# Performance work log

Measured on AMD Instinct MI355X. Metric: run time of the kernel, lower is better.

The kernel has to match this reference:

```python
import jax, jax.numpy as jnp
import numpy as np

B, T, D, H = 4, 1024, 1024, 16
DH = D // H
NEG_BIG = jnp.float32(-2.0**32 + 1)


def layer_norm(x, scale, bias, eps=1e-5):
    mean = jnp.mean(x, axis=-1, keepdims=True)
    var = jnp.mean(jnp.square(x - mean), axis=-1, keepdims=True)
    return (x - mean) * jax.lax.rsqrt(var + eps) * scale + bias


def setup_inputs() -> dict:
    key = jax.random.key(0)
    ks = jax.random.split(key, 10)
    s = 0.02
    x = jax.random.normal(ks[0], (B, T, D), jnp.float32)
    mask = jax.random.randint(ks[1], (B, T), 0, 2).astype(jnp.float32)
    return {
        "x": x,
        "mask": mask,
        "wq": jax.random.normal(ks[2], (D, D), jnp.float32) * s,
        "wk": jax.random.normal(ks[3], (D, D), jnp.float32) * s,
        "wv": jax.random.normal(ks[4], (D, D), jnp.float32) * s,
        "w1": jax.random.normal(ks[5], (D, D), jnp.float32) * s,
        "b1": jnp.zeros((D,), jnp.float32),
        "w2": jax.random.normal(ks[6], (D, D), jnp.float32) * s,
        "b2": jnp.zeros((D,), jnp.float32),
        "ln1_s": jnp.ones((D,), jnp.float32),
        "ln1_b": jnp.zeros((D,), jnp.float32),
        "ln2_s": jnp.ones((D,), jnp.float32),
        "ln2_b": jnp.zeros((D,), jnp.float32),
        "ln3_s": jnp.ones((D,), jnp.float32),
        "ln3_b": jnp.zeros((D,), jnp.float32),
    }


def _mask_enc(x, mask, wq, wk, wv, w1, b1, w2, b2,
              ln1_s, ln1_b, ln2_s, ln2_b, ln3_s, ln3_b):
    b, t, d = x.shape
    # --- multi-head attention (hand-rolled, matches torch split/cat trick) ---
    Q = (x @ wq).reshape(b, t, H, DH).transpose(0, 2, 1, 3)  # [B,H,T,dh]
    K = (x @ wk).reshape(b, t, H, DH).transpose(0, 2, 1, 3)
    V = (x @ wv).reshape(b, t, H, DH).transpose(0, 2, 1, 3)
    scores = jnp.einsum('bhqd,bhkd->bhqk', Q, K) / jnp.sqrt(jnp.float32(DH))
    # key padding mask from sign of |K| row sums
    key_m = jnp.sign(jnp.sum(jnp.abs(K), axis=-1))  # [B,H,T]
    scores = jnp.where(key_m[:, :, None, :] == 0, NEG_BIG, scores)
    # FORWARD direction: allowed where col_index > row_index (strict)
    idx = jnp.arange(t)
    allowed = (idx[None, :] > idx[:, None]).astype(scores.dtype)  # [T,T]
    scores = scores + (1.0 - allowed) * (-10000.0)
    attn = jax.nn.softmax(scores, axis=-1)
    # post-softmax query mask multiply
    query_m = jnp.sign(jnp.sum(jnp.abs(Q), axis=-1))[:, :, :, None]  # [B,H,T,1]
    attn = attn * query_m
    out = jnp.einsum('bhqk,bhkd->bhqd', attn, V)
    out = out.transpose(0, 2, 1, 3).reshape(b, t, d)  # combine heads
    out = out * mask[:, :, None]
    # --- residual + layernorm wrapper (attention) ---
    h1 = layer_norm(x + out, ln1_s, ln1_b)
    # --- FFN + residual + layernorm ---
    ffn = jax.nn.relu(h1 @ w1 + b1) @ w2 + b2
    h2 = layer_norm(h1 + ffn, ln2_s, ln2_b)
    # --- output normalization ---
    return layer_norm(h2, ln3_s, ln3_b)


def reference(x, mask, wq, wk, wv, w1, b1, w2, b2,
              ln1_s, ln1_b, ln2_s, ln2_b, ln3_s, ln3_b):
    return _mask_enc(x, mask, wq, wk, wv, w1, b1, w2, b2,
                     ln1_s, ln1_b, ln2_s, ln2_b, ln3_s, ln3_b)
```

## Files before the change

kernel.cpp:

```cpp
#include <hip/hip_runtime.h>
#include <stdint.h>


#define B_  4
#define T_  1024
#define D_  1024
#define H_  16
#define DH_ 64

typedef __attribute__((ext_vector_type(8))) short short8;
typedef __attribute__((ext_vector_type(4))) float floatx4;

__device__ __forceinline__ unsigned short f2bf(float f) {
  union { float f; uint32_t u; } a; a.f = f;
  uint32_t r = a.u + 0x7FFFu + ((a.u >> 16) & 1u);
  return (unsigned short)(r >> 16);
}
__device__ __forceinline__ float bf2f(unsigned short u) {
  union { uint32_t u; float f; } a; a.u = ((uint32_t)u) << 16;
  return a.f;
}

#define GLD_LDS16(g, l) __builtin_amdgcn_global_load_lds( \
    (const __attribute__((address_space(1))) unsigned int*)(g), \
    (__attribute__((address_space(3))) unsigned int*)(l), 16, 0, 0)

__global__ __launch_bounds__(256)
void cast_x_kernel(const float4* __restrict__ x4, unsigned short* __restrict__ xb) {
  int idx = blockIdx.x * 256 + threadIdx.x;
  float4 v = x4[idx];
  union { uint2 u; unsigned short s[4]; } o;
  o.s[0] = f2bf(v.x); o.s[1] = f2bf(v.y); o.s[2] = f2bf(v.z); o.s[3] = f2bf(v.w);
  *(uint2*)&xb[(size_t)idx * 4] = o.u;
}

__global__ __launch_bounds__(256)
void transpose_cast_w(const float* __restrict__ w0, const float* __restrict__ w1,
                      const float* __restrict__ w2, const float* __restrict__ w3,
                      const float* __restrict__ w4, unsigned short* __restrict__ dst_all) {
  const int z = blockIdx.z;
  const float* src = (z == 0) ? w0 : (z == 1) ? w1 : (z == 2) ? w2 : (z == 3) ? w3 : w4;
  unsigned short* dst = dst_all + (size_t)z * D_ * D_;
  __shared__ __align__(16) unsigned short tile[64 * 72];
  const int t = threadIdx.x;
  const int k0 = blockIdx.y * 64, n0 = blockIdx.x * 64;
#pragma unroll
  for (int c = 0; c < 4; ++c) {
    int idx = c * 256 + t;
    int r = idx >> 4, cc = (idx & 15) << 2;
    float4 v = *(const float4*)&src[(size_t)(k0 + r) * D_ + n0 + cc];
    tile[(cc + 0) * 72 + r] = f2bf(v.x);
    tile[(cc + 1) * 72 + r] = f2bf(v.y);
    tile[(cc + 2) * 72 + r] = f2bf(v.z);
    tile[(cc + 3) * 72 + r] = f2bf(v.w);
  }
  __syncthreads();
  int rr = t >> 2, ck = (t & 3) << 4;
  uint4 v0 = *(const uint4*)&tile[rr * 72 + ck];
  uint4 v1 = *(const uint4*)&tile[rr * 72 + ck + 8];
  *(uint4*)&dst[(size_t)(n0 + rr) * D_ + k0 + ck] = v0;
  *(uint4*)&dst[(size_t)(n0 + rr) * D_ + k0 + ck + 8] = v1;
}

__global__ __launch_bounds__(256, 2)
void gemm_qkv(const unsigned short* __restrict__ A,
              const unsigned short* __restrict__ Bt,
              unsigned short* __restrict__ oQ, unsigned short* __restrict__ oK,
              unsigned short* __restrict__ oV) {
  const int K = 1024;
  __shared__ __align__(16) unsigned short As[128 * 32];
  __shared__ __align__(16) unsigned short Bs[128 * 32];
  const int t = threadIdx.x;
  const int lane = t & 63, w = t >> 6;
  const int quad = lane >> 4, lm = lane & 15;
  const int wm = w >> 1, wn = w & 1;
  const int m0 = blockIdx.y * 128, n0 = blockIdx.x * 128;
  const int arow = w * 32 + (lane >> 2), acol = (lane & 3) << 3;

  floatx4 acc[4][4];
#pragma unroll
  for (int i = 0; i < 4; ++i)
#pragma unroll
    for (int j = 0; j < 4; ++j) acc[i][j] = (floatx4){0.f, 0.f, 0.f, 0.f};

  for (int kt = 0; kt < K; kt += 32) {
    const unsigned short* ga = A + (size_t)(m0 + arow) * K + kt + acol;
    const unsigned short* gb = Bt + (size_t)(n0 + arow) * K + kt + acol;
    GLD_LDS16(ga, &As[(w * 32) * 32]);
    GLD_LDS16(ga + (size_t)16 * K, &As[(w * 32 + 16) * 32]);
    GLD_LDS16(gb, &Bs[(w * 32) * 32]);
    GLD_LDS16(gb + (size_t)16 * K, &Bs[(w * 32 + 16) * 32]);
    __syncthreads();
    short8 a[4], b[4];
#pragma unroll
    for (int i = 0; i < 4; ++i) a[i] = *(const short8*)&As[(wm * 64 + i * 16 + lm) * 32 + quad * 8];
#pragma unroll
    for (int j = 0; j < 4; ++j) b[j] = *(const short8*)&Bs[(wn * 64 + j * 16 + lm) * 32 + quad * 8];
#pragma unroll
    for (int i = 0; i < 4; ++i)
#pragma unroll
      for (int j = 0; j < 4; ++j)
        acc[i][j] = __builtin_amdgcn_mfma_f32_16x16x32_bf16(a[i], b[j], acc[i][j], 0, 0, 0);
    __syncthreads();
  }

#pragma unroll
  for (int i = 0; i < 4; ++i) {
    int gmb = m0 + wm * 64 + i * 16 + quad * 4;
#pragma unroll
    for (int j = 0; j < 4; ++j) {
      int gn = n0 + wn * 64 + j * 16 + lm;
      int which = gn >> 10, nn = gn & 1023, hh = nn >> 6, dd = nn & 63;
#pragma unroll
      for (int r = 0; r < 4; ++r) {
        int gm = gmb + r;
        int bb = gm >> 10, tt = gm & 1023;
        unsigned short v = f2bf(acc[i][j][r]);
        if (which == 2) {
          oV[(((size_t)bb * H_ + hh) * DH_ + dd) * T_ + tt] = v;
        } else {
          unsigned short* p = (which == 0) ? oQ : oK;
          p[(((size_t)bb * H_ + hh) * T_ + tt) * DH_ + dd] = v;
        }
      }
    }
  }
}

template <int MODE>
__global__ __launch_bounds__(256, 2)
void gemm_ffn(const unsigned short* __restrict__ A,
              const unsigned short* __restrict__ Bt,
              unsigned short* __restrict__ oBf, float* __restrict__ oF,
              const float* __restrict__ bias) {
  const int K = 1024, N = 1024;
  __shared__ __align__(16) unsigned short As[64 * 32];
  __shared__ __align__(16) unsigned short Bs[128 * 32];
  const int t = threadIdx.x;
  const int lane = t & 63, w = t >> 6;
  const int quad = lane >> 4, lm = lane & 15;
  const int wm = w >> 1, wn = w & 1;
  const int m0 = blockIdx.y * 64, n0 = blockIdx.x * 128;
  const int lrow = lane >> 2, lcol = (lane & 3) << 3;

  floatx4 acc[2][4];
#pragma unroll
  for (int i = 0; i < 2; ++i)
#pragma unroll
    for (int j = 0; j < 4; ++j) acc[i][j] = (floatx4){0.f, 0.f, 0.f, 0.f};

  for (int kt = 0; kt < K; kt += 32) {
    const unsigned short* ga = A + (size_t)(m0 + w * 16 + lrow) * K + kt + lcol;
    const unsigned short* gb = Bt + (size_t)(n0 + w * 32 + lrow) * K + kt + lcol;
    GLD_LDS16(ga, &As[(w * 16) * 32]);
    GLD_LDS16(gb, &Bs[(w * 32) * 32]);
    GLD_LDS16(gb + (size_t)16 * K, &Bs[(w * 32 + 16) * 32]);
    __syncthreads();
    short8 a[2], b[4];
#pragma unroll
    for (int i = 0; i < 2; ++i) a[i] = *(const short8*)&As[(wm * 32 + i * 16 + lm) * 32 + quad * 8];
#pragma unroll
    for (int j = 0; j < 4; ++j) b[j] = *(const short8*)&Bs[(wn * 64 + j * 16 + lm) * 32 + quad * 8];
#pragma unroll
    for (int i = 0; i < 2; ++i)
#pragma unroll
      for (int j = 0; j < 4; ++j)
        acc[i][j] = __builtin_amdgcn_mfma_f32_16x16x32_bf16(a[i], b[j], acc[i][j], 0, 0, 0);
    __syncthreads();
  }

#pragma unroll
  for (int i = 0; i < 2; ++i) {
    int gmb = m0 + wm * 32 + i * 16 + quad * 4;
#pragma unroll
    for (int j = 0; j < 4; ++j) {
      int gn = n0 + wn * 64 + j * 16 + lm;
      float bv = bias[gn];
#pragma unroll
      for (int r = 0; r < 4; ++r) {
        int gm = gmb + r;
        float v = acc[i][j][r] + bv;
        if (MODE == 1) {
          oBf[(size_t)gm * N + gn] = f2bf(fmaxf(v, 0.f));
        } else {
          oF[(size_t)gm * N + gn] = v;
        }
      }
    }
  }
}

__global__ __launch_bounds__(256, 2)
void flash_attn(const unsigned short* __restrict__ Qb,
                const unsigned short* __restrict__ Kb,
                const unsigned short* __restrict__ Vtg,
                const float* __restrict__ maskp,
                unsigned short* __restrict__ attn) {
  __shared__ __align__(16) unsigned short Pt[4][128 * 36];

  const int t = threadIdx.x;
  const int lane = t & 63, w = t >> 6;
  const int quad = lane >> 4, lm = lane & 15;

  const int bid = blockIdx.x;
  const int hi = bid >> 8, lo = bid & 255;
  const int qraw = lo & 7;
  const int qb = hi ? (7 - qraw) : qraw;
  const int hb = (lo >> 3) | (hi << 5);
  const int hh = hb & 15, bb = hb >> 4;
  const int q0 = qb << 7;

  const size_t headoff = ((size_t)bb * H_ + hh) * T_ * DH_;
  const unsigned short* Qh = Qb + headoff;
  const unsigned short* Kh = Kb + headoff;
  const unsigned short* Vh = Vtg + headoff;
  unsigned short* Ptw = &Pt[w][0];

  short8 qa[2][2];
#pragma unroll
  for (int rg = 0; rg < 2; ++rg)
#pragma unroll
    for (int ks = 0; ks < 2; ++ks)
      qa[rg][ks] = *(const short8*)(Qh + (size_t)(q0 + w * 32 + rg * 16 + lm) * 64 + ks * 32 + quad * 8);

  float lsum[2][4];
#pragma unroll
  for (int rg = 0; rg < 2; ++rg)
#pragma unroll
    for (int r = 0; r < 4; ++r) lsum[rg][r] = 0.f;
  floatx4 acc_o[2][4];
#pragma unroll
  for (int rg = 0; rg < 2; ++rg)
#pragma unroll
    for (int j = 0; j < 4; ++j) acc_o[rg][j] = (floatx4){0.f, 0.f, 0.f, 0.f};

  for (int kb = qb; kb < 8; ++kb) {
    const int k0 = kb * 128;
    const bool need_mask = (kb == qb);
    const unsigned short* Kblk = Kh + (size_t)k0 * 64;

#pragma unroll
    for (int j = 0; j < 8; ++j) {
      short8 b0 = *(const short8*)(Kblk + (size_t)(j * 16 + lm) * 64 + quad * 8);
      short8 b1 = *(const short8*)(Kblk + (size_t)(j * 16 + lm) * 64 + 32 + quad * 8);
      floatx4 s0 = (floatx4){0.f, 0.f, 0.f, 0.f};
      floatx4 s1 = (floatx4){0.f, 0.f, 0.f, 0.f};
      s0 = __builtin_amdgcn_mfma_f32_16x16x32_bf16(qa[0][0], b0, s0, 0, 0, 0);
      s0 = __builtin_amdgcn_mfma_f32_16x16x32_bf16(qa[0][1], b1, s0, 0, 0, 0);
      s1 = __builtin_amdgcn_mfma_f32_16x16x32_bf16(qa[1][0], b0, s1, 0, 0, 0);
      s1 = __builtin_amdgcn_mfma_f32_16x16x32_bf16(qa[1][1], b1, s1, 0, 0, 0);
      const int coll = j * 16 + lm;
#pragma unroll
      for (int rg = 0; rg < 2; ++rg) {
        floatx4 sv = rg ? s1 : s0;
        union { unsigned short s[4]; uint2 u; } pk;
#pragma unroll
        for (int r = 0; r < 4; ++r) {
          int rowl = w * 32 + rg * 16 + quad * 4 + r;
          float v = sv[r] * 0.125f;
          if (need_mask && coll <= rowl) v -= 10000.f;
          float p = __expf(v);
          lsum[rg][r] += p;
          pk.s[r] = f2bf(p);
        }
        *(uint2*)&Ptw[coll * 36 + rg * 16 + quad * 4] = pk.u;
      }
    }

    short8 vbf[4][4];
#pragma unroll
    for (int j2 = 0; j2 < 4; ++j2)
#pragma unroll
      for (int ks = 0; ks < 4; ++ks)
        vbf[j2][ks] = *(const short8*)(Vh + (size_t)(j2 * 16 + lm) * T_ + k0 + ks * 32 + quad * 8);
    short8 pa[2][4];
#pragma unroll
    for (int rg = 0; rg < 2; ++rg)
#pragma unroll
      for (int ks = 0; ks < 4; ++ks) {
        short8 tmp;
#pragma unroll
        for (int jj = 0; jj < 8; ++jj)
          tmp[jj] = (short)Ptw[(ks * 32 + quad * 8 + jj) * 36 + rg * 16 + lm];
        pa[rg][ks] = tmp;
      }
#pragma unroll
    for (int rg = 0; rg < 2; ++rg)
#pragma unroll
      for (int j2 = 0; j2 < 4; ++j2)
#pragma unroll
        for (int ks = 0; ks < 4; ++ks)
          acc_o[rg][j2] = __builtin_amdgcn_mfma_f32_16x16x32_bf16(pa[rg][ks], vbf[j2][ks], acc_o[rg][j2], 0, 0, 0);
  }

#pragma unroll
  for (int rg = 0; rg < 2; ++rg) {
#pragma unroll
    for (int r = 0; r < 4; ++r) {
      float l = lsum[rg][r];
      l += __shfl_xor(l, 1); l += __shfl_xor(l, 2);
      l += __shfl_xor(l, 4); l += __shfl_xor(l, 8);
      int tq = q0 + w * 32 + rg * 16 + quad * 4 + r;
      float sc = maskp[bb * T_ + tq] / l;
#pragma unroll
      for (int j2 = 0; j2 < 4; ++j2)
        attn[((size_t)(bb * T_ + tq)) * D_ + hh * 64 + j2 * 16 + lm] = f2bf(acc_o[rg][j2][r] * sc);
    }
  }
}

__global__ __launch_bounds__(256)
void last_row_kernel(const unsigned short* __restrict__ Qb,
                     const unsigned short* __restrict__ Kb,
                     const unsigned short* __restrict__ Vtg,
                     const float* __restrict__ maskp,
                     unsigned short* __restrict__ attn) {
  const int hh = blockIdx.x, bb = blockIdx.y;
  const size_t headoff = ((size_t)bb * H_ + hh) * T_ * DH_;
  const unsigned short* Qh = Qb + headoff;
  const unsigned short* Kh = Kb + headoff;
  const unsigned short* Vh = Vtg + headoff;
  __shared__ float qrow[64];
  __shared__ float ps[1024];
  __shared__ float red[256];
  const int t = threadIdx.x;
  if (t < 64) qrow[t] = bf2f(Qh[(size_t)1023 * 64 + t]);
  __syncthreads();
  float lp = 0.f;
#pragma unroll
  for (int c = 0; c < 4; ++c) {
    int key = c * 256 + t;
    const unsigned short* kr = Kh + (size_t)key * 64;
    float dot = 0.f;
#pragma unroll
    for (int d8 = 0; d8 < 8; ++d8) {
      union { uint4 q; unsigned short s[8]; } kk;
      kk.q = *(const uint4*)&kr[d8 * 8];
#pragma unroll
      for (int u = 0; u < 8; ++u) dot += qrow[d8 * 8 + u] * bf2f(kk.s[u]);
    }
    float p = __expf(dot * 0.125f);
    ps[key] = p;
    lp += p;
  }
  red[t] = lp;
  __syncthreads();
  for (int s = 128; s > 0; s >>= 1) {
    if (t < s) red[t] += red[t + s];
    __syncthreads();
  }
  float ltot = red[0];
  __syncthreads();
  const int d = t & 63, part = t >> 6;
  const unsigned short* vr = Vh + (size_t)d * T_ + part * 256;
  float acc = 0.f;
#pragma unroll
  for (int c = 0; c < 32; ++c) {
    union { uint4 q; unsigned short s[8]; } vv;
    vv.q = *(const uint4*)&vr[c * 8];
#pragma unroll
    for (int u = 0; u < 8; ++u) acc += ps[part * 256 + c * 8 + u] * bf2f(vv.s[u]);
  }
  red[t] = acc;
  __syncthreads();
  if (t < 64) {
    float tot = red[t] + red[t + 64] + red[t + 128] + red[t + 192];
    attn[((size_t)(bb * T_ + 1023)) * D_ + hh * 64 + t] =
        f2bf(tot / ltot * maskp[bb * T_ + 1023]);
  }
}

__global__ __launch_bounds__(256)
void ln_res_kernel(const float* __restrict__ xa, const unsigned short* __restrict__ attn,
                   const float* __restrict__ sc, const float* __restrict__ bi,
                   float* __restrict__ h, unsigned short* __restrict__ hb) {
  const int row = blockIdx.x, t = threadIdx.x;
  const int lane = t & 63, wid = t >> 6;
  size_t base = (size_t)row * D_ + t * 4;
  float4 a = *(const float4*)&xa[base];
  union { uint2 u; unsigned short s[4]; } au;
  au.u = *(const uint2*)&attn[base];
  float v0 = a.x + bf2f(au.s[0]), v1 = a.y + bf2f(au.s[1]);
  float v2 = a.z + bf2f(au.s[2]), v3 = a.w + bf2f(au.s[3]);
  float s1 = v0 + v1 + v2 + v3;
  float s2 = v0 * v0 + v1 * v1 + v2 * v2 + v3 * v3;
#pragma unroll
  for (int off = 32; off; off >>= 1) { s1 += __shfl_down(s1, off); s2 += __shfl_down(s2, off); }
  __shared__ float r1[4], r2[4];
  if (lane == 0) { r1[wid] = s1; r2[wid] = s2; }
  __syncthreads();
  s1 = r1[0] + r1[1] + r1[2] + r1[3];
  s2 = r2[0] + r2[1] + r2[2] + r2[3];
  float mean = s1 * (1.f / 1024.f);
  float var = s2 * (1.f / 1024.f) - mean * mean;
  float rstd = rsqrtf(var + 1e-5f);
  float4 sv = *(const float4*)&sc[t * 4];
  float4 bv = *(const float4*)&bi[t * 4];
  float o0 = (v0 - mean) * rstd * sv.x + bv.x;
  float o1 = (v1 - mean) * rstd * sv.y + bv.y;
  float o2 = (v2 - mean) * rstd * sv.z + bv.z;
  float o3 = (v3 - mean) * rstd * sv.w + bv.w;
  float4 ov = {o0, o1, o2, o3};
  *(float4*)&h[base] = ov;
  union { uint2 u; unsigned short s[4]; } ob;
  ob.s[0] = f2bf(o0); ob.s[1] = f2bf(o1); ob.s[2] = f2bf(o2); ob.s[3] = f2bf(o3);
  *(uint2*)&hb[base] = ob.u;
}

__global__ __launch_bounds__(256)
void ln_double_kernel(const float* __restrict__ h1, const float* __restrict__ ffn,
                      const float* __restrict__ s2c, const float* __restrict__ b2c,
                      const float* __restrict__ s3c, const float* __restrict__ b3c,
                      float* __restrict__ out) {
  const int row = blockIdx.x, t = threadIdx.x;
  const int lane = t & 63, wid = t >> 6;
  size_t base = (size_t)row * D_ + t * 4;
  float4 a = *(const float4*)&h1[base];
  float4 b = *(const float4*)&ffn[base];
  float v0 = a.x + b.x, v1 = a.y + b.y, v2 = a.z + b.z, v3 = a.w + b.w;
  float s1 = v0 + v1 + v2 + v3;
  float s2 = v0 * v0 + v1 * v1 + v2 * v2 + v3 * v3;
#pragma unroll
  for (int off = 32; off; off >>= 1) { s1 += __shfl_down(s1, off); s2 += __shfl_down(s2, off); }
  __shared__ float ra[4], rb[4], rc[4], rd[4];
  if (lane == 0) { ra[wid] = s1; rb[wid] = s2; }
  __syncthreads();
  s1 = ra[0] + ra[1] + ra[2] + ra[3];
  s2 = rb[0] + rb[1] + rb[2] + rb[3];
  float mean = s1 * (1.f / 1024.f);
  float var = s2 * (1.f / 1024.f) - mean * mean;
  float rstd = rsqrtf(var + 1e-5f);
  float4 sv = *(const float4*)&s2c[t * 4];
  float4 bv = *(const float4*)&b2c[t * 4];
  float o0 = (v0 - mean) * rstd * sv.x + bv.x;
  float o1 = (v1 - mean) * rstd * sv.y + bv.y;
  float o2 = (v2 - mean) * rstd * sv.z + bv.z;
  float o3 = (v3 - mean) * rstd * sv.w + bv.w;
  float u1 = o0 + o1 + o2 + o3;
  float u2 = o0 * o0 + o1 * o1 + o2 * o2 + o3 * o3;
#pragma unroll
  for (int off = 32; off; off >>= 1) { u1 += __shfl_down(u1, off); u2 += __shfl_down(u2, off); }
  if (lane == 0) { rc[wid] = u1; rd[wid] = u2; }
  __syncthreads();
  u1 = rc[0] + rc[1] + rc[2] + rc[3];
  u2 = rd[0] + rd[1] + rd[2] + rd[3];
  float mean2 = u1 * (1.f / 1024.f);
  float var2 = u2 * (1.f / 1024.f) - mean2 * mean2;
  float rstd2 = rsqrtf(var2 + 1e-5f);
  float4 s3v = *(const float4*)&s3c[t * 4];
  float4 b3v = *(const float4*)&b3c[t * 4];
  float4 fo;
  fo.x = (o0 - mean2) * rstd2 * s3v.x + b3v.x;
  fo.y = (o1 - mean2) * rstd2 * s3v.y + b3v.y;
  fo.z = (o2 - mean2) * rstd2 * s3v.z + b3v.z;
  fo.w = (o3 - mean2) * rstd2 * s3v.w + b3v.w;
  *(float4*)&out[base] = fo;
}

extern "C" void kernel_launch(void* const* d_in, const int* in_sizes, int n_in,
                              void* d_out, int out_size, void* d_ws, size_t ws_size,
                              hipStream_t stream) {
  (void)in_sizes; (void)n_in; (void)out_size; (void)ws_size;
  const float* x   = (const float*)d_in[0];
  const float* msk = (const float*)d_in[1];
  const float* wq  = (const float*)d_in[2];
  const float* wk  = (const float*)d_in[3];
  const float* wv  = (const float*)d_in[4];
  const float* w1  = (const float*)d_in[5];
  const float* b1  = (const float*)d_in[6];
  const float* w2  = (const float*)d_in[7];
  const float* b2  = (const float*)d_in[8];
  const float* l1s = (const float*)d_in[9];
  const float* l1b = (const float*)d_in[10];
  const float* l2s = (const float*)d_in[11];
  const float* l2b = (const float*)d_in[12];
  const float* l3s = (const float*)d_in[13];
  const float* l3b = (const float*)d_in[14];
  float* outp = (float*)d_out;

  char* ws = (char*)d_ws;
  unsigned short* xb   = (unsigned short*)(ws);
  unsigned short* wt   = (unsigned short*)(ws + ((size_t)8  << 20));
  unsigned short* Qb   = (unsigned short*)(ws + ((size_t)18 << 20));
  unsigned short* Kb   = (unsigned short*)(ws + ((size_t)26 << 20));
  unsigned short* Vtg  = (unsigned short*)(ws + ((size_t)34 << 20));
  unsigned short* attn = (unsigned short*)(ws + ((size_t)42 << 20));
  float* h1            = (float*)(ws + ((size_t)50 << 20));
  unsigned short* h1b  = (unsigned short*)(ws + ((size_t)18 << 20));
  unsigned short* gb   = (unsigned short*)(ws + ((size_t)26 << 20));
  float* ffn           = (float*)(ws + ((size_t)34 << 20));

  cast_x_kernel<<<4096, 256, 0, stream>>>((const float4*)x, xb);
  transpose_cast_w<<<dim3(16, 16, 5), 256, 0, stream>>>(wq, wk, wv, w1, w2, wt);
  gemm_qkv<<<dim3(24, 32), 256, 0, stream>>>(xb, wt, Qb, Kb, Vtg);
  flash_attn<<<512, 256, 0, stream>>>(Qb, Kb, Vtg, msk, attn);
  last_row_kernel<<<dim3(16, 4), 256, 0, stream>>>(Qb, Kb, Vtg, msk, attn);
  ln_res_kernel<<<4096, 256, 0, stream>>>(x, attn, l1s, l1b, h1, h1b);
  gemm_ffn<1><<<dim3(8, 64), 256, 0, stream>>>(h1b, wt + (size_t)3 * 1024 * 1024, gb, nullptr, b1);
  gemm_ffn<2><<<dim3(8, 64), 256, 0, stream>>>(gb, wt + (size_t)4 * 1024 * 1024, nullptr, ffn, b2);
  ln_double_kernel<<<4096, 256, 0, stream>>>(h1, ffn, l2s, l2b, l3s, l3b, outp);
}
```

Measured before the change: 267.3 us.

## Keep attention probabilities in registers via transposed S and fp16 PV MFMA

```diff
diff --git a/kernel.cpp b/kernel.cpp
--- a/kernel.cpp
+++ b/kernel.cpp
@@ -10,6 +10,7 @@
 
 typedef __attribute__((ext_vector_type(8))) short short8;
 typedef __attribute__((ext_vector_type(4))) float floatx4;
+typedef __attribute__((ext_vector_type(4))) _Float16 half4;
 
 __device__ __forceinline__ unsigned short f2bf(float f) {
   union { float f; uint32_t u; } a; a.f = f;
@@ -66,7 +67,7 @@
 void gemm_qkv(const unsigned short* __restrict__ A,
               const unsigned short* __restrict__ Bt,
               unsigned short* __restrict__ oQ, unsigned short* __restrict__ oK,
-              unsigned short* __restrict__ oV) {
+              _Float16* __restrict__ oV) {
   const int K = 1024;
   __shared__ __align__(16) unsigned short As[128 * 32];
   __shared__ __align__(16) unsigned short Bs[128 * 32];
@@ -115,12 +116,12 @@
       for (int r = 0; r < 4; ++r) {
         int gm = gmb + r;
         int bb = gm >> 10, tt = gm & 1023;
-        unsigned short v = f2bf(acc[i][j][r]);
+        float v = acc[i][j][r];
         if (which == 2) {
-          oV[(((size_t)bb * H_ + hh) * DH_ + dd) * T_ + tt] = v;
+          oV[(((size_t)bb * H_ + hh) * DH_ + dd) * T_ + tt] = (_Float16)v;
         } else {
           unsigned short* p = (which == 0) ? oQ : oK;
-          p[(((size_t)bb * H_ + hh) * T_ + tt) * DH_ + dd] = v;
+          p[(((size_t)bb * H_ + hh) * T_ + tt) * DH_ + dd] = f2bf(v);
         }
       }
     }
@@ -190,14 +191,12 @@
   }
 }
 
-__global__ __launch_bounds__(256, 2)
+__global__ __launch_bounds__(256, 4)
 void flash_attn(const unsigned short* __restrict__ Qb,
                 const unsigned short* __restrict__ Kb,
-                const unsigned short* __restrict__ Vtg,
+                const _Float16* __restrict__ Vtg,
                 const float* __restrict__ maskp,
                 unsigned short* __restrict__ attn) {
-  __shared__ __align__(16) unsigned short Pt[4][128 * 36];
-
   const int t = threadIdx.x;
   const int lane = t & 63, w = t >> 6;
   const int quad = lane >> 4, lm = lane & 15;
@@ -213,26 +212,23 @@
   const size_t headoff = ((size_t)bb * H_ + hh) * T_ * DH_;
   const unsigned short* Qh = Qb + headoff;
   const unsigned short* Kh = Kb + headoff;
-  const unsigned short* Vh = Vtg + headoff;
-  unsigned short* Ptw = &Pt[w][0];
-
-  short8 qa[2][2];
-#pragma unroll
-  for (int rg = 0; rg < 2; ++rg)
+  const _Float16* Vh = Vtg + headoff;
+
+  short8 qf[2][2];
+#pragma unroll
+  for (int qg = 0; qg < 2; ++qg)
 #pragma unroll
     for (int ks = 0; ks < 2; ++ks)
-      qa[rg][ks] = *(const short8*)(Qh + (size_t)(q0 + w * 32 + rg * 16 + lm) * 64 + ks * 32 + quad * 8);
-
-  float lsum[2][4];
-#pragma unroll
-  for (int rg = 0; rg < 2; ++rg)
-#pragma unroll
-    for (int r = 0; r < 4; ++r) lsum[rg][r] = 0.f;
-  floatx4 acc_o[2][4];
-#pragma unroll
-  for (int rg = 0; rg < 2; ++rg)
-#pragma unroll
-    for (int j = 0; j < 4; ++j) acc_o[rg][j] = (floatx4){0.f, 0.f, 0.f, 0.f};
+      qf[qg][ks] = *(const short8*)(Qh + (size_t)(q0 + w * 32 + qg * 16 + lm) * 64 + ks * 32 + quad * 8);
+
+  float lsum[2] = {0.f, 0.f};
+  floatx4 acc[2][4];
+#pragma unroll
+  for (int qg = 0; qg < 2; ++qg)
+#pragma unroll
+    for (int j2 = 0; j2 < 4; ++j2) acc[qg][j2] = (floatx4){0.f, 0.f, 0.f, 0.f};
+
+  const int qglob0 = q0 + w * 32 + lm;
 
   for (int kb = qb; kb < 8; ++kb) {
     const int k0 = kb * 128;
@@ -241,70 +237,51 @@
 
 #pragma unroll
     for (int j = 0; j < 8; ++j) {
-      short8 b0 = *(const short8*)(Kblk + (size_t)(j * 16 + lm) * 64 + quad * 8);
-      short8 b1 = *(const short8*)(Kblk + (size_t)(j * 16 + lm) * 64 + 32 + quad * 8);
-      floatx4 s0 = (floatx4){0.f, 0.f, 0.f, 0.f};
-      floatx4 s1 = (floatx4){0.f, 0.f, 0.f, 0.f};
-      s0 = __builtin_amdgcn_mfma_f32_16x16x32_bf16(qa[0][0], b0, s0, 0, 0, 0);
-      s0 = __builtin_amdgcn_mfma_f32_16x16x32_bf16(qa[0][1], b1, s0, 0, 0, 0);
-      s1 = __builtin_amdgcn_mfma_f32_16x16x32_bf16(qa[1][0], b0, s1, 0, 0, 0);
-      s1 = __builtin_amdgcn_mfma_f32_16x16x32_bf16(qa[1][1], b1, s1, 0, 0, 0);
-      const int coll = j * 16 + lm;
-#pragma unroll
-      for (int rg = 0; rg < 2; ++rg) {
-        floatx4 sv = rg ? s1 : s0;
-        union { unsigned short s[4]; uint2 u; } pk;
+      short8 kf0 = *(const short8*)(Kblk + (size_t)(j * 16 + lm) * 64 + quad * 8);
+      short8 kf1 = *(const short8*)(Kblk + (size_t)(j * 16 + lm) * 64 + 32 + quad * 8);
+      floatx4 st[2];
+#pragma unroll
+      for (int qg = 0; qg < 2; ++qg) {
+        floatx4 z = (floatx4){0.f, 0.f, 0.f, 0.f};
+        z = __builtin_amdgcn_mfma_f32_16x16x32_bf16(kf0, qf[qg][0], z, 0, 0, 0);
+        st[qg] = __builtin_amdgcn_mfma_f32_16x16x32_bf16(kf1, qf[qg][1], z, 0, 0, 0);
+      }
+      half4 pa[2];
+#pragma unroll
+      for (int qg = 0; qg < 2; ++qg) {
+        const int qg_q = qglob0 + qg * 16;
 #pragma unroll
         for (int r = 0; r < 4; ++r) {
-          int rowl = w * 32 + rg * 16 + quad * 4 + r;
-          float v = sv[r] * 0.125f;
-          if (need_mask && coll <= rowl) v -= 10000.f;
+          int kg = k0 + j * 16 + quad * 4 + r;
+          float v = st[qg][r] * 0.125f;
+          if (need_mask && kg <= qg_q) v -= 10000.f;
           float p = __expf(v);
-          lsum[rg][r] += p;
-          pk.s[r] = f2bf(p);
+          lsum[qg] += p;
+          pa[qg][r] = (_Float16)p;
         }
-        *(uint2*)&Ptw[coll * 36 + rg * 16 + quad * 4] = pk.u;
+      }
+#pragma unroll
+      for (int j2 = 0; j2 < 4; ++j2) {
+        half4 vb = *(const half4*)(Vh + (size_t)(j2 * 16 + lm) * T_ + k0 + j * 16 + quad * 4);
+        acc[0][j2] = __builtin_amdgcn_mfma_f32_16x16x16f16(pa[0], vb, acc[0][j2], 0, 0, 0);
+        acc[1][j2] = __builtin_amdgcn_mfma_f32_16x16x16f16(pa[1], vb, acc[1][j2], 0, 0, 0);
       }
     }
-
-    short8 vbf[4][4];
-#pragma unroll
-    for (int j2 = 0; j2 < 4; ++j2)
-#pragma unroll
-      for (int ks = 0; ks < 4; ++ks)
-        vbf[j2][ks] = *(const short8*)(Vh + (size_t)(j2 * 16 + lm) * T_ + k0 + ks * 32 + quad * 8);
-    short8 pa[2][4];
-#pragma unroll
-    for (int rg = 0; rg < 2; ++rg)
-#pragma unroll
-      for (int ks = 0; ks < 4; ++ks) {
-        short8 tmp;
-#pragma unroll
-        for (int jj = 0; jj < 8; ++jj)
-          tmp[jj] = (short)Ptw[(ks * 32 + quad * 8 + jj) * 36 + rg * 16 + lm];
-        pa[rg][ks] = tmp;
-      }
-#pragma unroll
-    for (int rg = 0; rg < 2; ++rg)
+  }
+
+#pragma unroll
+  for (int qg = 0; qg < 2; ++qg) {
+    float l = lsum[qg];
+    l += __shfl_xor(l, 16);
+    l += __shfl_xor(l, 32);
+    float s = maskp[bb * T_ + qglob0 + qg * 16] / l;
+#pragma unroll
+    for (int r = 0; r < 4; ++r) {
+      float bsc = __shfl(s, quad * 4 + r);
+      int tq = q0 + w * 32 + qg * 16 + quad * 4 + r;
 #pragma unroll
       for (int j2 = 0; j2 < 4; ++j2)
-#pragma unroll
-        for (int ks = 0; ks < 4; ++ks)
-          acc_o[rg][j2] = __builtin_amdgcn_mfma_f32_16x16x32_bf16(pa[rg][ks], vbf[j2][ks], acc_o[rg][j2], 0, 0, 0);
-  }
-
-#pragma unroll
-  for (int rg = 0; rg < 2; ++rg) {
-#pragma unroll
-    for (int r = 0; r < 4; ++r) {
-      float l = lsum[rg][r];
-      l += __shfl_xor(l, 1); l += __shfl_xor(l, 2);
-      l += __shfl_xor(l, 4); l += __shfl_xor(l, 8);
-      int tq = q0 + w * 32 + rg * 16 + quad * 4 + r;
-      float sc = maskp[bb * T_ + tq] / l;
-#pragma unroll
-      for (int j2 = 0; j2 < 4; ++j2)
-        attn[((size_t)(bb * T_ + tq)) * D_ + hh * 64 + j2 * 16 + lm] = f2bf(acc_o[rg][j2][r] * sc);
+        attn[((size_t)(bb * T_ + tq)) * D_ + hh * 64 + j2 * 16 + lm] = f2bf(acc[qg][j2][r] * bsc);
     }
   }
 }
@@ -312,14 +289,14 @@
 __global__ __launch_bounds__(256)
 void last_row_kernel(const unsigned short* __restrict__ Qb,
                      const unsigned short* __restrict__ Kb,
-                     const unsigned short* __restrict__ Vtg,
+                     const _Float16* __restrict__ Vtg,
                      const float* __restrict__ maskp,
                      unsigned short* __restrict__ attn) {
   const int hh = blockIdx.x, bb = blockIdx.y;
   const size_t headoff = ((size_t)bb * H_ + hh) * T_ * DH_;
   const unsigned short* Qh = Qb + headoff;
   const unsigned short* Kh = Kb + headoff;
-  const unsigned short* Vh = Vtg + headoff;
+  const _Float16* Vh = Vtg + headoff;
   __shared__ float qrow[64];
   __shared__ float ps[1024];
   __shared__ float red[256];
@@ -352,14 +329,14 @@
   float ltot = red[0];
   __syncthreads();
   const int d = t & 63, part = t >> 6;
-  const unsigned short* vr = Vh + (size_t)d * T_ + part * 256;
+  const _Float16* vr = Vh + (size_t)d * T_ + part * 256;
   float acc = 0.f;
 #pragma unroll
   for (int c = 0; c < 32; ++c) {
-    union { uint4 q; unsigned short s[8]; } vv;
+    union { uint4 q; _Float16 h[8]; } vv;
     vv.q = *(const uint4*)&vr[c * 8];
 #pragma unroll
-    for (int u = 0; u < 8; ++u) acc += ps[part * 256 + c * 8 + u] * bf2f(vv.s[u]);
+    for (int u = 0; u < 8; ++u) acc += ps[part * 256 + c * 8 + u] * (float)vv.h[u];
   }
   red[t] = acc;
   __syncthreads();
@@ -483,7 +460,7 @@
   unsigned short* wt   = (unsigned short*)(ws + ((size_t)8  << 20));
   unsigned short* Qb   = (unsigned short*)(ws + ((size_t)18 << 20));
   unsigned short* Kb   = (unsigned short*)(ws + ((size_t)26 << 20));
-  unsigned short* Vtg  = (unsigned short*)(ws + ((size_t)34 << 20));
+  _Float16*       Vtg  = (_Float16*)(ws + ((size_t)34 << 20));
   unsigned short* attn = (unsigned short*)(ws + ((size_t)42 << 20));
   float* h1            = (float*)(ws + ((size_t)50 << 20));
   unsigned short* h1b  = (unsigned short*)(ws + ((size_t)18 << 20));
```

Result: slower. 289.9 us (+8.5%).
